# Kernel tuning notes

Measured on AMD Instinct MI355X. Metric: run time of the kernel, lower is better.

Reference implementation:

```python
import jax, jax.numpy as jnp
import numpy as np

THR = 0.2          # config['thr']
BORDER_RM = 2      # config['border_rm']
TEMP = 0.1         # config['dsmax_temperature']


def setup_inputs() -> dict:
    key = jax.random.key(0)
    k0, k1 = jax.random.split(key)
    N, C = 2, 256
    h0c, w0c, h1c, w1c = 60, 80, 60, 80
    return {
        "feat_c0": jax.random.normal(k0, (N, h0c * w0c, C), dtype=jnp.float32),
        "feat_c1": jax.random.normal(k1, (N, h1c * w1c, C), dtype=jnp.float32),
        "h0c": h0c, "w0c": w0c, "h1c": h1c, "w1c": w1c,
    }


def _valid_1d(n: int, b: int):
    # True in the interior [b, n-b), False on the border — matches mask_border writes
    return jnp.zeros((n,), dtype=bool).at[b:n - b].set(True)


def reference(feat_c0, feat_c1, h0c, w0c, h1c, w1c):
    N, L, C = feat_c0.shape
    S = feat_c1.shape[1]
    scale = 1.0 / (C ** 0.5)
    f0 = feat_c0 * scale
    f1 = feat_c1 * scale

    # similarity + dual softmax  -> conf_matrix [N, L, S]
    sim = jnp.einsum('nlc,nsc->nls', f0, f1) / TEMP
    conf = jax.nn.softmax(sim, axis=1) * jax.nn.softmax(sim, axis=2)

    # threshold + border removal (mask_border, vectorized as an interior mask)
    mask = conf > THR
    b = BORDER_RM
    border = (_valid_1d(h0c, b)[:, None, None, None]
              & _valid_1d(w0c, b)[None, :, None, None]
              & _valid_1d(h1c, b)[None, None, :, None]
              & _valid_1d(w1c, b)[None, None, None, :])  # [h0c,w0c,h1c,w1c]
    mask = (mask.reshape(N, h0c, w0c, h1c, w1c) & border[None]).reshape(N, L, S)

    # mutual nearest neighbor
    mask = mask \
        & (conf == conf.max(axis=2, keepdims=True)) \
        & (conf == conf.max(axis=1, keepdims=True))

    # match extraction, expressed densely (static shapes for jit):
    # mask_v[b,i] = row i of pair b has a match; j_ids its column; mconf its confidence
    mask_v = mask.any(axis=2)                               # [N, L]
    j_ids = jnp.argmax(mask, axis=2)                        # [N, L] (first True)
    mconf = jnp.take_along_axis(conf, j_ids[:, :, None], axis=2)[..., 0]
    mconf = jnp.where(mask_v, mconf, 0.0)                   # [N, L]

    # coarse keypoint coords for matched columns: (x, y) = (j % w1c, j // w1c)
    mkpts1_c = jnp.stack([j_ids % w1c, j_ids // w1c], axis=-1)  # [N, L, 2]

    return conf, mask_v, j_ids, mkpts1_c, mconf
```

## Files before the change

### kernel.cpp

```cpp
#include <hip/hip_runtime.h>

typedef _Float16 half8 __attribute__((ext_vector_type(8)));
typedef float f32x4 __attribute__((ext_vector_type(4)));

#define NB 2
#define LS 4800
#define CCH 256
#define W0 80
#define W1 80
#define THRV 0.2f
#define SQS 0.19764235376052370f

#define TN  38
#define TNM 19
#define PADL 4864
#define NWG (TN * TNM * NB)

#define OF_RST  0
#define OF_CST  19200
#define OF_RWM  38400
#define OF_CAND 48000
#define OF_CLM  57600
#define OF_PROW 67200
#define OF_PCOL (67200 + 739328)
#define OF_AH   (67200 + 2*739328)
#define OF_BH   (OF_AH + 1228800)

#define O_MASKV 46080000ull
#define O_JIDS  46089600ull
#define O_MKPT  46099200ull
#define O_MCONF 46118400ull

__device__ __forceinline__ void load_lds16(const void* g, void* l) {
    __builtin_amdgcn_global_load_lds((const __attribute__((address_space(1))) void*)g,
                                     (__attribute__((address_space(3))) void*)l, 16, 0, 0);
}

__device__ __forceinline__ void swizzle_ids(int& n, int& by, int& bx) {
    const int orig = ((int)blockIdx.z * TNM + (int)blockIdx.y) * TN + (int)blockIdx.x;
    const int xcd = orig & 7, t = orig >> 3;
    const int wg = (xcd < 4 ? xcd * 181 : 724 + (xcd - 4) * 180) + t;
    n = wg / (TN * TNM);
    const int rem = wg % (TN * TNM);
    by = rem / TN; bx = rem % TN;
}

__global__ __launch_bounds__(256) void conv_half(const float* __restrict__ A,
                                                 const float* __restrict__ B,
                                                 float* __restrict__ ws) {
    const int which = blockIdx.y;
    const float* src = which ? B : A;
    _Float16* dst = (_Float16*)(ws + (which ? OF_BH : OF_AH));
    const int idx = blockIdx.x * 256 + threadIdx.x;
    const float4 v = ((const float4*)src)[idx];
    union { _Float16 h[4]; uint2 u; } p;
    p.h[0] = (_Float16)(v.x * SQS);
    p.h[1] = (_Float16)(v.y * SQS);
    p.h[2] = (_Float16)(v.z * SQS);
    p.h[3] = (_Float16)(v.w * SQS);
    ((uint2*)dst)[idx] = p.u;
}

__device__ __forceinline__ void gemm_core(const _Float16* __restrict__ Ah,
                                          const _Float16* __restrict__ Bh,
                                          _Float16* smA, _Float16* smB,
                                          const int bx, const int by,
                                          const int tid, f32x4 (&acc)[4][4]) {
    const int lane = tid & 63, w = tid >> 6;
    const int wx = w & 1, wy = w >> 1;
    const int m = lane & 15, quad = lane >> 4;
    const int rr = lane >> 2;
    const int q = (lane & 3) ^ ((lane >> 3) & 3);

    const _Float16* ga[2];
    const _Float16* gb0;
    {
#pragma unroll
        for (int i = 0; i < 2; i++) {
            const int c = w * 2 + i;
            int gra = by * 256 + c * 16 + rr; gra = gra < LS ? gra : LS - 1;
            ga[i] = Ah + (size_t)gra * CCH + q * 8;
        }
        int grb = bx * 128 + w * 16 + rr; grb = grb < LS ? grb : LS - 1;
        gb0 = Bh + (size_t)grb * CCH + q * 8;
    }

#pragma unroll
    for (int i = 0; i < 2; i++) load_lds16(ga[i], &smA[(w * 2 + i) * 512]);
    load_lds16(gb0, &smB[w * 512]);

    for (int kt = 0; kt < 8; kt++) {
        __syncthreads();
        const int curA = (kt & 1) * 8192, curB = (kt & 1) * 4096;
        if (kt < 7) {
            const int ko = (kt + 1) * 32;
#pragma unroll
            for (int i = 0; i < 2; i++)
                load_lds16(ga[i] + ko, &smA[(8192 - curA) + (w * 2 + i) * 512]);
            load_lds16(gb0 + ko, &smB[(4096 - curB) + w * 512]);
        }
        half8 Af[4], Bf[4];
#pragma unroll
        for (int a = 0; a < 4; a++) {
            const int rl = wy * 64 + a * 16 + m;
            const int sl = rl * 4 + (quad ^ ((rl >> 1) & 3));
            Af[a] = *(const half8*)&smA[curA + sl * 8];
        }
#pragma unroll
        for (int b = 0; b < 4; b++) {
            const int cl = wx * 64 + b * 16 + m;
            const int sl = cl * 4 + (quad ^ ((cl >> 1) & 3));
            Bf[b] = *(const half8*)&smB[curB + sl * 8];
        }
#pragma unroll
        for (int a = 0; a < 4; a++)
#pragma unroll
            for (int b = 0; b < 4; b++)
                acc[a][b] = __builtin_amdgcn_mfma_f32_16x16x32_f16(Af[a], Bf[b], acc[a][b], 0, 0, 0);
    }
    __syncthreads();
}

__global__ __launch_bounds__(512, 4) void gemm_stats(float* __restrict__ ws) {
    __shared__ __align__(16) union {
        struct { _Float16 A[2][8192]; _Float16 B[2][4096]; } st;
        struct { float rs[256][2][2]; float cs[128][4][2]; } red;
    } sm;
    int n, by, bx;
    swizzle_ids(n, by, bx);
    const _Float16* Ah = (const _Float16*)(ws + OF_AH) + (size_t)n * LS * CCH;
    const _Float16* Bh = (const _Float16*)(ws + OF_BH) + (size_t)n * LS * CCH;
    const int tid = threadIdx.x;
    const int lane = tid & 63, w = tid >> 6;
    const int wx = w & 1, wy = w >> 1;
    const int m = lane & 15, quad = lane >> 4;

    f32x4 acc[4][4];
    {
        f32x4 z = {0.f, 0.f, 0.f, 0.f};
#pragma unroll
        for (int a = 0; a < 4; a++)
#pragma unroll
            for (int b = 0; b < 4; b++) acc[a][b] = z;
    }
    gemm_core(Ah, Bh, &sm.st.A[0][0], &sm.st.B[0][0], bx, by, tid, acc);

    const int l0 = by * 256, s0 = bx * 128;
    bool bval[4];
#pragma unroll
    for (int b = 0; b < 4; b++) bval[b] = (s0 + wx * 64 + b * 16 + m) < LS;

    float T = -1e30f;
#pragma unroll
    for (int a = 0; a < 4; a++)
#pragma unroll
        for (int reg = 0; reg < 4; reg++) {
            if ((l0 + wy * 64 + a * 16 + quad * 4 + reg) < LS) {
#pragma unroll
                for (int b = 0; b < 4; b++)
                    if (bval[b]) T = fmaxf(T, acc[a][b][reg]);
            }
        }
#pragma unroll
    for (int d = 1; d < 64; d <<= 1) T = fmaxf(T, __shfl_xor(T, d, 64));

#pragma unroll
    for (int a = 0; a < 4; a++)
#pragma unroll
        for (int reg = 0; reg < 4; reg++) {
            const bool rv = (l0 + wy * 64 + a * 16 + quad * 4 + reg) < LS;
#pragma unroll
            for (int b = 0; b < 4; b++)
                acc[a][b][reg] = (rv && bval[b]) ? __expf(acc[a][b][reg] - T) : 0.f;
        }

#pragma unroll
    for (int a = 0; a < 4; a++)
#pragma unroll
        for (int reg = 0; reg < 4; reg++) {
            float s = acc[a][0][reg] + acc[a][1][reg] + acc[a][2][reg] + acc[a][3][reg];
#pragma unroll
            for (int d = 1; d < 16; d <<= 1) s += __shfl_xor(s, d, 64);
            if (m == 0) {
                const int rl = wy * 64 + a * 16 + quad * 4 + reg;
                sm.red.rs[rl][wx][0] = T; sm.red.rs[rl][wx][1] = s;
            }
        }
#pragma unroll
    for (int b = 0; b < 4; b++) {
        float s = 0.f;
#pragma unroll
        for (int a = 0; a < 4; a++)
#pragma unroll
            for (int reg = 0; reg < 4; reg++) s += acc[a][b][reg];
        s += __shfl_xor(s, 16, 64);
        s += __shfl_xor(s, 32, 64);
        if (quad == 0) {
            const int cl = wx * 64 + b * 16 + m;
            sm.red.cs[cl][wy][0] = T; sm.red.cs[cl][wy][1] = s;
        }
    }
    __syncthreads();
    if (tid < 256) {
        const float m0 = sm.red.rs[tid][0][0], v0 = sm.red.rs[tid][0][1];
        const float m1 = sm.red.rs[tid][1][0], v1 = sm.red.rs[tid][1][1];
        const float nm = fmaxf(m0, m1);
        const float s = v0 * __expf(m0 - nm) + v1 * __expf(m1 - nm);
        ((float2*)(ws + OF_PROW))[((size_t)n * PADL + l0 + tid) * TN + bx] = make_float2(nm, s);
    } else if (tid < 384) {
        const int t = tid - 256;
        float M = sm.red.cs[t][0][0], S = sm.red.cs[t][0][1];
#pragma unroll
        for (int k = 1; k < 4; k++) {
            const float mo = sm.red.cs[t][k][0], so = sm.red.cs[t][k][1];
            const float nm = fmaxf(M, mo);
            S = S * __expf(M - nm) + so * __expf(mo - nm);
            M = nm;
        }
        ((float2*)(ws + OF_PCOL))[((size_t)n * PADL + s0 + t) * TNM + by] = make_float2(M, S);
    }
}

__global__ __launch_bounds__(256) void combine_stats(float* __restrict__ ws) {
    const int idx = blockIdx.x * 256 + threadIdx.x;
    const int half_ = idx >= 9600;
    const int i = idx - half_ * 9600;
    const int n = i / LS, r = i % LS;
    float M = -1e30f, S = 0.f;
    if (!half_) {
        const float2* P = (const float2*)(ws + OF_PROW) + ((size_t)n * PADL + r) * TN;
        for (int b = 0; b < TN; b++) {
            const float2 p = P[b];
            const float nm = fmaxf(M, p.x);
            S = S * __expf(M - nm) + p.y * __expf(p.x - nm);
            M = nm;
        }
        ((float2*)(ws + OF_RST))[n * LS + r] = make_float2(M, 1.0f / S);
    } else {
        const float2* P = (const float2*)(ws + OF_PCOL) + ((size_t)n * PADL + r) * TNM;
        for (int b = 0; b < TNM; b++) {
            const float2 p = P[b];
            const float nm = fmaxf(M, p.x);
            S = S * __expf(M - nm) + p.y * __expf(p.x - nm);
            M = nm;
        }
        ((float2*)(ws + OF_CST))[n * LS + r] = make_float2(M, 1.0f / S);
    }
}

__global__ __launch_bounds__(512, 4) void gemm_conf(float* __restrict__ out,
                                                    float* __restrict__ ws) {
    __shared__ __align__(16) union {
        struct { _Float16 A[2][8192]; _Float16 B[2][4096]; } st;
        struct { float rst[256][2]; float cst[128][2];
                 float rsv[256][2][2]; float csv[128][4]; } ep;
    } sm;
    int n, by, bx;
    swizzle_ids(n, by, bx);
    const _Float16* Ah = (const _Float16*)(ws + OF_AH) + (size_t)n * LS * CCH;
    const _Float16* Bh = (const _Float16*)(ws + OF_BH) + (size_t)n * LS * CCH;
    const int tid = threadIdx.x;
    const int lane = tid & 63, w = tid >> 6;
    const int wx = w & 1, wy = w >> 1;
    const int m = lane & 15, quad = lane >> 4;

    f32x4 acc[4][4];
    {
        f32x4 z = {0.f, 0.f, 0.f, 0.f};
#pragma unroll
        for (int a = 0; a < 4; a++)
#pragma unroll
            for (int b = 0; b < 4; b++) acc[a][b] = z;
    }
    gemm_core(Ah, Bh, &sm.st.A[0][0], &sm.st.B[0][0], bx, by, tid, acc);

    const int l0 = by * 256, s0 = bx * 128;
    if (tid < 256) {
        int r = l0 + tid; r = r < LS ? r : LS - 1;
        const float2 v = ((const float2*)(ws + OF_RST))[n * LS + r];
        sm.ep.rst[tid][0] = v.x; sm.ep.rst[tid][1] = v.y;
    } else if (tid < 384) {
        const int t = tid - 256;
        int c = s0 + t; c = c < LS ? c : LS - 1;
        const float2 v = ((const float2*)(ws + OF_CST))[n * LS + c];
        sm.ep.cst[t][0] = v.x; sm.ep.cst[t][1] = v.y;
    }
    __syncthreads();

    float* On = out + (size_t)n * LS * LS;
    float colm[4] = {-1.f, -1.f, -1.f, -1.f};
    bool bval[4]; int gc4[4]; float cmx[4], csi[4];
#pragma unroll
    for (int b = 0; b < 4; b++) {
        const int cl = wx * 64 + b * 16 + m;
        gc4[b] = s0 + cl;
        bval[b] = gc4[b] < LS;
        cmx[b] = sm.ep.cst[cl][0]; csi[b] = sm.ep.cst[cl][1];
    }
#pragma unroll
    for (int a = 0; a < 4; a++) {
#pragma unroll
        for (int reg = 0; reg < 4; reg++) {
            const int rl = wy * 64 + a * 16 + quad * 4 + reg;
            const int gr = l0 + rl;
            const float rm = sm.ep.rst[rl][0], rsi = sm.ep.rst[rl][1];
            const bool rv = gr < LS;
            float bestv = -1.f; int besti = 0;
#pragma unroll
            for (int b = 0; b < 4; b++) {
                const float c = __expf(2.f * acc[a][b][reg] - rm - cmx[b]) * (rsi * csi[b]);
                if (rv && bval[b]) {
                    __builtin_nontemporal_store(c, &On[(size_t)gr * LS + gc4[b]]);
                    if (c > bestv) { bestv = c; besti = gc4[b]; }
                    colm[b] = fmaxf(colm[b], c);
                }
            }
#pragma unroll
            for (int d = 1; d < 16; d <<= 1) {
                const float ov = __shfl_xor(bestv, d, 64);
                const int oi = __shfl_xor(besti, d, 64);
                if (ov > bestv || (ov == bestv && oi < besti)) { bestv = ov; besti = oi; }
            }
            if (m == 0) {
                sm.ep.rsv[rl][wx][0] = bestv;
                sm.ep.rsv[rl][wx][1] = __int_as_float(besti);
            }
        }
    }
#pragma unroll
    for (int b = 0; b < 4; b++) {
        float v = colm[b];
        v = fmaxf(v, __shfl_xor(v, 16, 64));
        v = fmaxf(v, __shfl_xor(v, 32, 64));
        if (quad == 0) sm.ep.csv[wx * 64 + b * 16 + m][wy] = v;
    }
    __syncthreads();
    if (tid < 256) {
        const float v0 = sm.ep.rsv[tid][0][0]; const int i0 = __float_as_int(sm.ep.rsv[tid][0][1]);
        const float v1 = sm.ep.rsv[tid][1][0]; const int i1 = __float_as_int(sm.ep.rsv[tid][1][1]);
        float bv; int bi;
        if (v0 > v1 || (v0 == v1 && i0 <= i1)) { bv = v0; bi = i0; } else { bv = v1; bi = i1; }
        ((float2*)(ws + OF_PROW))[((size_t)n * PADL + l0 + tid) * TN + bx] =
            make_float2(bv, __int_as_float(bi));
    } else if (tid < 384) {
        const int t = tid - 256;
        const float v = fmaxf(fmaxf(sm.ep.csv[t][0], sm.ep.csv[t][1]),
                              fmaxf(sm.ep.csv[t][2], sm.ep.csv[t][3]));
        (ws + OF_PCOL)[((size_t)n * PADL + s0 + t) * TNM + by] = v;
    }
}

__global__ __launch_bounds__(256) void combine_max(float* __restrict__ ws) {
    const int idx = blockIdx.x * 256 + threadIdx.x;
    const int half_ = idx >= 9600;
    const int i = idx - half_ * 9600;
    const int n = i / LS, r = i % LS;
    if (!half_) {
        const float2* P = (const float2*)(ws + OF_PROW) + ((size_t)n * PADL + r) * TN;
        float bv = -2.f; int bi = 0;
        for (int b = 0; b < TN; b++) {
            const float2 p = P[b];
            const int pi = __float_as_int(p.y);
            if (p.x > bv || (p.x == bv && pi < bi)) { bv = p.x; bi = pi; }
        }
        ws[OF_RWM + i] = bv;
        ((int*)ws)[OF_CAND + i] = bi;
    } else {
        const float* P = ws + OF_PCOL + ((size_t)n * PADL + r) * TNM;
        float v = -2.f;
        for (int b = 0; b < TNM; b++) v = fmaxf(v, P[b]);
        ws[OF_CLM + i] = v;
    }
}

__global__ __launch_bounds__(256) void match_pass(const float* __restrict__ ws,
                                                  float* __restrict__ out) {
    const int idx = blockIdx.x * 256 + threadIdx.x;
    if (idx >= NB * LS) return;
    const int n = idx / LS, l = idx % LS;
    const float rwm = ws[OF_RWM + idx];
    const int cand = ((const int*)ws)[OF_CAND + idx];
    const float clm = ws[OF_CLM + n * LS + cand];
    const int y0 = l / W0, x0 = l % W0;
    const int y1 = cand / W1, x1 = cand % W1;
    const bool b0 = (y0 >= 2 && y0 < 58 && x0 >= 2 && x0 < 78);
    const bool b1 = (y1 >= 2 && y1 < 58 && x1 >= 2 && x1 < 78);
    const bool matched = (rwm > THRV) && b0 && b1 && (rwm == clm);
    const int j = matched ? cand : 0;
    out[O_MASKV + idx] = matched ? 1.f : 0.f;
    out[O_JIDS + idx] = (float)j;
    out[O_MKPT + (size_t)idx * 2 + 0] = (float)(j % W1);
    out[O_MKPT + (size_t)idx * 2 + 1] = (float)(j / W1);
    out[O_MCONF + idx] = matched ? rwm : 0.f;
}

extern "C" void kernel_launch(void* const* d_in, const int* in_sizes, int n_in,
                              void* d_out, int out_size, void* d_ws, size_t ws_size,
                              hipStream_t stream) {
    const float* f0 = (const float*)d_in[0];
    const float* f1 = (const float*)d_in[1];
    float* out = (float*)d_out;
    float* ws = (float*)d_ws;

    conv_half<<<dim3(2400, 2), 256, 0, stream>>>(f0, f1, ws);
    gemm_stats<<<dim3(TN, TNM, NB), 512, 0, stream>>>(ws);
    combine_stats<<<75, 256, 0, stream>>>(ws);
    gemm_conf<<<dim3(TN, TNM, NB), 512, 0, stream>>>(out, ws);
    combine_max<<<75, 256, 0, stream>>>(ws);
    match_pass<<<38, 256, 0, stream>>>(ws, out);
}
```

Baseline: 310.6 us.

## Store raw similarity once and stream-normalize instead of recomputing GEMM

Drops the second GEMM pass. The first GEMM now writes raw similarity logits into the output buffer, and a new streaming kernel reads them back, applies the dual-softmax normalization in place, and computes per-row argmax and per-block column maxima. A simpler column-combine kernel replaces the old partial-max combine. The trade is cheaper compute for an extra full read and write of the 4800x4800 fp32 matrix per batch. The streaming kernel also runs on only 300 blocks, which may limit achievable bandwidth.

```diff
diff --git a/kernel.cpp b/kernel.cpp
--- a/kernel.cpp
+++ b/kernel.cpp
@@ -14,7 +14,8 @@
 #define TN  38
 #define TNM 19
 #define PADL 4864
-#define NWG (TN * TNM * NB)
+#define NROWB 32
+#define NPB   150
 
 #define OF_RST  0
 #define OF_CST  19200
@@ -23,6 +24,7 @@
 #define OF_CLM  57600
 #define OF_PROW 67200
 #define OF_PCOL (67200 + 739328)
+#define OF_CMAXP OF_PROW
 #define OF_AH   (67200 + 2*739328)
 #define OF_BH   (OF_AH + 1228800)
 
@@ -121,7 +123,8 @@
     __syncthreads();
 }
 
-__global__ __launch_bounds__(512, 4) void gemm_stats(float* __restrict__ ws) {
+__global__ __launch_bounds__(512, 4) void gemm_sim(float* __restrict__ out,
+                                                   float* __restrict__ ws) {
     __shared__ __align__(16) union {
         struct { _Float16 A[2][8192]; _Float16 B[2][4096]; } st;
         struct { float rs[256][2][2]; float cs[128][4][2]; } red;
@@ -146,9 +149,25 @@
     gemm_core(Ah, Bh, &sm.st.A[0][0], &sm.st.B[0][0], bx, by, tid, acc);
 
     const int l0 = by * 256, s0 = bx * 128;
-    bool bval[4];
-#pragma unroll
-    for (int b = 0; b < 4; b++) bval[b] = (s0 + wx * 64 + b * 16 + m) < LS;
+    bool bval[4]; int gc4[4];
+#pragma unroll
+    for (int b = 0; b < 4; b++) {
+        gc4[b] = s0 + wx * 64 + b * 16 + m;
+        bval[b] = gc4[b] < LS;
+    }
+
+    float* On = out + (size_t)n * LS * LS;
+#pragma unroll
+    for (int a = 0; a < 4; a++)
+#pragma unroll
+        for (int reg = 0; reg < 4; reg++) {
+            const int gr = l0 + wy * 64 + a * 16 + quad * 4 + reg;
+            if (gr < LS) {
+#pragma unroll
+                for (int b = 0; b < 4; b++)
+                    if (bval[b]) On[(size_t)gr * LS + gc4[b]] = acc[a][b][reg];
+            }
+        }
 
     float T = -1e30f;
 #pragma unroll
@@ -248,129 +267,86 @@
     }
 }
 
-__global__ __launch_bounds__(512, 4) void gemm_conf(float* __restrict__ out,
-                                                    float* __restrict__ ws) {
-    __shared__ __align__(16) union {
-        struct { _Float16 A[2][8192]; _Float16 B[2][4096]; } st;
-        struct { float rst[256][2]; float cst[128][2];
-                 float rsv[256][2][2]; float csv[128][4]; } ep;
-    } sm;
-    int n, by, bx;
-    swizzle_ids(n, by, bx);
-    const _Float16* Ah = (const _Float16*)(ws + OF_AH) + (size_t)n * LS * CCH;
-    const _Float16* Bh = (const _Float16*)(ws + OF_BH) + (size_t)n * LS * CCH;
+__global__ __launch_bounds__(256) void stream_conf(float* __restrict__ out,
+                                                   float* __restrict__ ws) {
+    const int n = blockIdx.y, rb = blockIdx.x;
     const int tid = threadIdx.x;
-    const int lane = tid & 63, w = tid >> 6;
-    const int wx = w & 1, wy = w >> 1;
-    const int m = lane & 15, quad = lane >> 4;
-
-    f32x4 acc[4][4];
-    {
-        f32x4 z = {0.f, 0.f, 0.f, 0.f};
-#pragma unroll
-        for (int a = 0; a < 4; a++)
-#pragma unroll
-            for (int b = 0; b < 4; b++) acc[a][b] = z;
-    }
-    gemm_core(Ah, Bh, &sm.st.A[0][0], &sm.st.B[0][0], bx, by, tid, acc);
-
-    const int l0 = by * 256, s0 = bx * 128;
-    if (tid < 256) {
-        int r = l0 + tid; r = r < LS ? r : LS - 1;
-        const float2 v = ((const float2*)(ws + OF_RST))[n * LS + r];
-        sm.ep.rst[tid][0] = v.x; sm.ep.rst[tid][1] = v.y;
-    } else if (tid < 384) {
-        const int t = tid - 256;
-        int c = s0 + t; c = c < LS ? c : LS - 1;
-        const float2 v = ((const float2*)(ws + OF_CST))[n * LS + c];
-        sm.ep.cst[t][0] = v.x; sm.ep.cst[t][1] = v.y;
-    }
-    __syncthreads();
-
-    float* On = out + (size_t)n * LS * LS;
-    float colm[4] = {-1.f, -1.f, -1.f, -1.f};
-    bool bval[4]; int gc4[4]; float cmx[4], csi[4];
-#pragma unroll
-    for (int b = 0; b < 4; b++) {
-        const int cl = wx * 64 + b * 16 + m;
-        gc4[b] = s0 + cl;
-        bval[b] = gc4[b] < LS;
-        cmx[b] = sm.ep.cst[cl][0]; csi[b] = sm.ep.cst[cl][1];
-    }
-#pragma unroll
-    for (int a = 0; a < 4; a++) {
-#pragma unroll
-        for (int reg = 0; reg < 4; reg++) {
-            const int rl = wy * 64 + a * 16 + quad * 4 + reg;
-            const int gr = l0 + rl;
-            const float rm = sm.ep.rst[rl][0], rsi = sm.ep.rst[rl][1];
-            const bool rv = gr < LS;
-            float bestv = -1.f; int besti = 0;
-#pragma unroll
-            for (int b = 0; b < 4; b++) {
-                const float c = __expf(2.f * acc[a][b][reg] - rm - cmx[b]) * (rsi * csi[b]);
-                if (rv && bval[b]) {
-                    __builtin_nontemporal_store(c, &On[(size_t)gr * LS + gc4[b]]);
-                    if (c > bestv) { bestv = c; besti = gc4[b]; }
-                    colm[b] = fmaxf(colm[b], c);
+    __shared__ float Lv[16][256];
+    __shared__ int   Li[16][256];
+    __shared__ float Mv[16][16];
+    __shared__ int   Mi[16][16];
+
+    float cmv[19], csiv[19], cmax[19];
+#pragma unroll
+    for (int j = 0; j < 19; j++) {
+        const int s = tid + j * 256;
+        cmax[j] = 0.f;
+        if (s < LS) {
+            const float2 v = ((const float2*)(ws + OF_CST))[n * LS + s];
+            cmv[j] = v.x; csiv[j] = v.y;
+        } else { cmv[j] = 0.f; csiv[j] = 0.f; }
+    }
+
+    float* base = out + ((size_t)n * LS + rb * NROWB) * LS;
+    for (int ch = 0; ch < 2; ch++) {
+        for (int r16 = 0; r16 < 16; r16++) {
+            const int r = ch * 16 + r16;
+            const float2 rs = ((const float2*)(ws + OF_RST))[n * LS + rb * NROWB + r];
+            float* row = base + (size_t)r * LS;
+            float lmax = -1.f; int lidx = 0;
+#pragma unroll
+            for (int j = 0; j < 19; j++) {
+                const int s = tid + j * 256;
+                if (s < LS) {
+                    const float x = row[s];
+                    const float c = __expf(2.f * x - rs.x - cmv[j]) * (rs.y * csiv[j]);
+                    __builtin_nontemporal_store(c, &row[s]);
+                    cmax[j] = fmaxf(cmax[j], c);
+                    if (c > lmax) { lmax = c; lidx = s; }
                 }
             }
-#pragma unroll
-            for (int d = 1; d < 16; d <<= 1) {
-                const float ov = __shfl_xor(bestv, d, 64);
-                const int oi = __shfl_xor(besti, d, 64);
-                if (ov > bestv || (ov == bestv && oi < besti)) { bestv = ov; besti = oi; }
-            }
-            if (m == 0) {
-                sm.ep.rsv[rl][wx][0] = bestv;
-                sm.ep.rsv[rl][wx][1] = __int_as_float(besti);
-            }
-        }
-    }
-#pragma unroll
-    for (int b = 0; b < 4; b++) {
-        float v = colm[b];
-        v = fmaxf(v, __shfl_xor(v, 16, 64));
-        v = fmaxf(v, __shfl_xor(v, 32, 64));
-        if (quad == 0) sm.ep.csv[wx * 64 + b * 16 + m][wy] = v;
-    }
-    __syncthreads();
-    if (tid < 256) {
-        const float v0 = sm.ep.rsv[tid][0][0]; const int i0 = __float_as_int(sm.ep.rsv[tid][0][1]);
-        const float v1 = sm.ep.rsv[tid][1][0]; const int i1 = __float_as_int(sm.ep.rsv[tid][1][1]);
-        float bv; int bi;
-        if (v0 > v1 || (v0 == v1 && i0 <= i1)) { bv = v0; bi = i0; } else { bv = v1; bi = i1; }
-        ((float2*)(ws + OF_PROW))[((size_t)n * PADL + l0 + tid) * TN + bx] =
-            make_float2(bv, __int_as_float(bi));
-    } else if (tid < 384) {
-        const int t = tid - 256;
-        const float v = fmaxf(fmaxf(sm.ep.csv[t][0], sm.ep.csv[t][1]),
-                              fmaxf(sm.ep.csv[t][2], sm.ep.csv[t][3]));
-        (ws + OF_PCOL)[((size_t)n * PADL + s0 + t) * TNM + by] = v;
-    }
-}
-
-__global__ __launch_bounds__(256) void combine_max(float* __restrict__ ws) {
+            Lv[r16][tid] = lmax; Li[r16][tid] = lidx;
+        }
+        __syncthreads();
+        {
+            const int r = tid >> 4, p = tid & 15;
+            float bv = -2.f; int bi = 0;
+            for (int k = 0; k < 16; k++) {
+                const float v = Lv[r][p * 16 + k]; const int ii = Li[r][p * 16 + k];
+                if (v > bv || (v == bv && ii < bi)) { bv = v; bi = ii; }
+            }
+            Mv[r][p] = bv; Mi[r][p] = bi;
+        }
+        __syncthreads();
+        if (tid < 16) {
+            float bv = -2.f; int bi = 0;
+            for (int p = 0; p < 16; p++) {
+                const float v = Mv[tid][p]; const int ii = Mi[tid][p];
+                if (v > bv || (v == bv && ii < bi)) { bv = v; bi = ii; }
+            }
+            const int gr = n * LS + rb * NROWB + ch * 16 + tid;
+            ws[OF_RWM + gr] = bv;
+            ((int*)ws)[OF_CAND + gr] = bi;
+        }
+        __syncthreads();
+    }
+
+#pragma unroll
+    for (int j = 0; j < 19; j++) {
+        const int s = tid + j * 256;
+        if (s < LS) ws[OF_CMAXP + ((size_t)n * NPB + rb) * LS + s] = cmax[j];
+    }
+}
+
+__global__ __launch_bounds__(256) void combine_col(float* __restrict__ ws) {
     const int idx = blockIdx.x * 256 + threadIdx.x;
-    const int half_ = idx >= 9600;
-    const int i = idx - half_ * 9600;
-    const int n = i / LS, r = i % LS;
-    if (!half_) {
-        const float2* P = (const float2*)(ws + OF_PROW) + ((size_t)n * PADL + r) * TN;
-        float bv = -2.f; int bi = 0;
-        for (int b = 0; b < TN; b++) {
-            const float2 p = P[b];
-            const int pi = __float_as_int(p.y);
-            if (p.x > bv || (p.x == bv && pi < bi)) { bv = p.x; bi = pi; }
-        }
-        ws[OF_RWM + i] = bv;
-        ((int*)ws)[OF_CAND + i] = bi;
-    } else {
-        const float* P = ws + OF_PCOL + ((size_t)n * PADL + r) * TNM;
-        float v = -2.f;
-        for (int b = 0; b < TNM; b++) v = fmaxf(v, P[b]);
-        ws[OF_CLM + i] = v;
-    }
+    if (idx >= NB * LS) return;
+    const int n = idx / LS, c = idx % LS;
+    const float* P = ws + OF_CMAXP + (size_t)n * NPB * LS + c;
+    float v = -2.f;
+#pragma unroll 4
+    for (int p = 0; p < NPB; p++) v = fmaxf(v, P[(size_t)p * LS]);
+    ws[OF_CLM + idx] = v;
 }
 
 __global__ __launch_bounds__(256) void match_pass(const float* __restrict__ ws,
@@ -403,9 +379,9 @@
     float* ws = (float*)d_ws;
 
     conv_half<<<dim3(2400, 2), 256, 0, stream>>>(f0, f1, ws);
-    gemm_stats<<<dim3(TN, TNM, NB), 512, 0, stream>>>(ws);
+    gemm_sim<<<dim3(TN, TNM, NB), 512, 0, stream>>>(out, ws);
     combine_stats<<<75, 256, 0, stream>>>(ws);
-    gemm_conf<<<dim3(TN, TNM, NB), 512, 0, stream>>>(out, ws);
-    combine_max<<<75, 256, 0, stream>>>(ws);
+    stream_conf<<<dim3(NPB, NB), 256, 0, stream>>>(out, ws);
+    combine_col<<<38, 256, 0, stream>>>(ws);
     match_pass<<<38, 256, 0, stream>>>(ws, out);
 }
```

Result: slower. 353.6 us (+13.8%).

## Restructure GEMM tiles to 64x128 with full-K LDS A and register-streamed B

Applied to the files above, without the earlier changes.

The GEMM tile changes from 256x128 to 64x128. The whole K extent of A is staged once in LDS, and each wave streams its B fragments straight from global memory into registers with a three-deep prefetch, which removes the per-k-step barriers and the B LDS staging. Column partial statistics now go into scratch space in the output buffer instead of workspace. The column max is reduced with atomicMax into a zeroed buffer, so the separate column-combine pass is dropped, and the non-temporal conf stores become plain stores. The smaller tile means four times as many workgroups and more redundant B reads per output element, in exchange for less synchronization and better occupancy.

```diff
diff --git a/kernel.cpp b/kernel.cpp
--- a/kernel.cpp
+++ b/kernel.cpp
@@ -11,10 +11,10 @@
 #define THRV 0.2f
 #define SQS 0.19764235376052370f
 
-#define TN  38
-#define TNM 19
-#define PADL 4864
-#define NWG (TN * TNM * NB)
+#define TBX 38
+#define TBY 75
+#define PIMG (TBX * TBY)
+#define NWG  (PIMG * NB)
 
 #define OF_RST  0
 #define OF_CST  19200
@@ -22,9 +22,8 @@
 #define OF_CAND 48000
 #define OF_CLM  57600
 #define OF_PROW 67200
-#define OF_PCOL (67200 + 739328)
-#define OF_AH   (67200 + 2*739328)
-#define OF_BH   (OF_AH + 1228800)
+#define OF_AH   796800
+#define OF_BH   2025600
 
 #define O_MASKV 46080000ull
 #define O_JIDS  46089600ull
@@ -37,12 +36,12 @@
 }
 
 __device__ __forceinline__ void swizzle_ids(int& n, int& by, int& bx) {
-    const int orig = ((int)blockIdx.z * TNM + (int)blockIdx.y) * TN + (int)blockIdx.x;
+    const int orig = ((int)blockIdx.z * TBY + (int)blockIdx.y) * TBX + (int)blockIdx.x;
     const int xcd = orig & 7, t = orig >> 3;
-    const int wg = (xcd < 4 ? xcd * 181 : 724 + (xcd - 4) * 180) + t;
-    n = wg / (TN * TNM);
-    const int rem = wg % (TN * TNM);
-    by = rem / TN; bx = rem % TN;
+    const int wg = (xcd < 4 ? xcd * 713 : 2852 + (xcd - 4) * 712) + t;
+    n = wg / PIMG;
+    const int rem = wg % PIMG;
+    by = rem / TBX; bx = rem % TBX;
 }
 
 __global__ __launch_bounds__(256) void conv_half(const float* __restrict__ A,
@@ -61,175 +60,181 @@
     ((uint2*)dst)[idx] = p.u;
 }
 
-__device__ __forceinline__ void gemm_core(const _Float16* __restrict__ Ah,
-                                          const _Float16* __restrict__ Bh,
-                                          _Float16* smA, _Float16* smB,
-                                          const int bx, const int by,
-                                          const int tid, f32x4 (&acc)[4][4]) {
-    const int lane = tid & 63, w = tid >> 6;
-    const int wx = w & 1, wy = w >> 1;
-    const int m = lane & 15, quad = lane >> 4;
-    const int rr = lane >> 2;
-    const int q = (lane & 3) ^ ((lane >> 3) & 3);
-
-    const _Float16* ga[2];
-    const _Float16* gb0;
-    {
-#pragma unroll
-        for (int i = 0; i < 2; i++) {
-            const int c = w * 2 + i;
-            int gra = by * 256 + c * 16 + rr; gra = gra < LS ? gra : LS - 1;
-            ga[i] = Ah + (size_t)gra * CCH + q * 8;
-        }
-        int grb = bx * 128 + w * 16 + rr; grb = grb < LS ? grb : LS - 1;
-        gb0 = Bh + (size_t)grb * CCH + q * 8;
-    }
-
-#pragma unroll
-    for (int i = 0; i < 2; i++) load_lds16(ga[i], &smA[(w * 2 + i) * 512]);
-    load_lds16(gb0, &smB[w * 512]);
-
+__device__ __forceinline__ void stage_A(const _Float16* __restrict__ Ah,
+                                        _Float16* smA, const int by, const int tid) {
+#pragma unroll
+    for (int i = 0; i < 4; i++) {
+        const int s = i * 512 + tid;
+        const int slice = s >> 8, rem = s & 255, row = rem >> 2, j = rem & 3;
+        const int q = j ^ ((row >> 1) & 3);
+        load_lds16(Ah + (size_t)(by * 64 + row) * CCH + slice * 32 + q * 8, smA + s * 8);
+    }
+}
+
+__device__ __forceinline__ void kloop(const _Float16* smA,
+                                      const _Float16* __restrict__ Bh,
+                                      const int colb, const int wrow,
+                                      const int m, const int quad,
+                                      f32x4 (&acc)[2][2]) {
+    const _Float16* bp0 = Bh + (size_t)(colb + m) * CCH + quad * 8;
+    const _Float16* bp1 = bp0 + 16 * CCH;
+    half8 Bs[3][2], Af[2][2];
+    Bs[0][0] = *(const half8*)bp0;
+    Bs[0][1] = *(const half8*)bp1;
+    Bs[1][0] = *(const half8*)(bp0 + 32);
+    Bs[1][1] = *(const half8*)(bp1 + 32);
+#pragma unroll
+    for (int a = 0; a < 2; a++) {
+        const int rl = wrow * 32 + a * 16 + m;
+        const int sl = rl * 4 + (quad ^ ((rl >> 1) & 3));
+        Af[0][a] = *(const half8*)&smA[sl * 8];
+    }
+#pragma unroll
     for (int kt = 0; kt < 8; kt++) {
-        __syncthreads();
-        const int curA = (kt & 1) * 8192, curB = (kt & 1) * 4096;
+        if (kt < 6) {
+            Bs[(kt + 2) % 3][0] = *(const half8*)(bp0 + (kt + 2) * 32);
+            Bs[(kt + 2) % 3][1] = *(const half8*)(bp1 + (kt + 2) * 32);
+        }
         if (kt < 7) {
-            const int ko = (kt + 1) * 32;
-#pragma unroll
-            for (int i = 0; i < 2; i++)
-                load_lds16(ga[i] + ko, &smA[(8192 - curA) + (w * 2 + i) * 512]);
-            load_lds16(gb0 + ko, &smB[(4096 - curB) + w * 512]);
-        }
-        half8 Af[4], Bf[4];
-#pragma unroll
-        for (int a = 0; a < 4; a++) {
-            const int rl = wy * 64 + a * 16 + m;
-            const int sl = rl * 4 + (quad ^ ((rl >> 1) & 3));
-            Af[a] = *(const half8*)&smA[curA + sl * 8];
-        }
-#pragma unroll
-        for (int b = 0; b < 4; b++) {
-            const int cl = wx * 64 + b * 16 + m;
-            const int sl = cl * 4 + (quad ^ ((cl >> 1) & 3));
-            Bf[b] = *(const half8*)&smB[curB + sl * 8];
-        }
-#pragma unroll
-        for (int a = 0; a < 4; a++)
-#pragma unroll
-            for (int b = 0; b < 4; b++)
-                acc[a][b] = __builtin_amdgcn_mfma_f32_16x16x32_f16(Af[a], Bf[b], acc[a][b], 0, 0, 0);
-    }
-    __syncthreads();
-}
-
-__global__ __launch_bounds__(512, 4) void gemm_stats(float* __restrict__ ws) {
-    __shared__ __align__(16) union {
-        struct { _Float16 A[2][8192]; _Float16 B[2][4096]; } st;
-        struct { float rs[256][2][2]; float cs[128][4][2]; } red;
-    } sm;
+#pragma unroll
+            for (int a = 0; a < 2; a++) {
+                const int rl = wrow * 32 + a * 16 + m;
+                const int sl = (kt + 1) * 256 + rl * 4 + (quad ^ ((rl >> 1) & 3));
+                Af[(kt + 1) & 1][a] = *(const half8*)&smA[sl * 8];
+            }
+        }
+#pragma unroll
+        for (int a = 0; a < 2; a++)
+#pragma unroll
+            for (int b = 0; b < 2; b++)
+                acc[a][b] = __builtin_amdgcn_mfma_f32_16x16x32_f16(Af[kt & 1][a], Bs[kt % 3][b], acc[a][b], 0, 0, 0);
+    }
+}
+
+__global__ __launch_bounds__(512, 4) void gemm_stats(float* __restrict__ out,
+                                                     float* __restrict__ ws) {
+    __shared__ __align__(16) _Float16 smA[16384];
+    __shared__ float rs[64][4][2];
+    __shared__ float cs[128][2][2];
     int n, by, bx;
     swizzle_ids(n, by, bx);
     const _Float16* Ah = (const _Float16*)(ws + OF_AH) + (size_t)n * LS * CCH;
     const _Float16* Bh = (const _Float16*)(ws + OF_BH) + (size_t)n * LS * CCH;
     const int tid = threadIdx.x;
     const int lane = tid & 63, w = tid >> 6;
-    const int wx = w & 1, wy = w >> 1;
+    const int wrow = w >> 2, wcol = w & 3;
     const int m = lane & 15, quad = lane >> 4;
 
-    f32x4 acc[4][4];
+    stage_A(Ah, smA, by, tid);
+    __syncthreads();
+
+    const int colb = bx * 128 + wcol * 32;
+    const bool bvalid = colb < LS;
+    f32x4 acc[2][2];
     {
         f32x4 z = {0.f, 0.f, 0.f, 0.f};
-#pragma unroll
-        for (int a = 0; a < 4; a++)
-#pragma unroll
-            for (int b = 0; b < 4; b++) acc[a][b] = z;
-    }
-    gemm_core(Ah, Bh, &sm.st.A[0][0], &sm.st.B[0][0], bx, by, tid, acc);
-
-    const int l0 = by * 256, s0 = bx * 128;
-    bool bval[4];
-#pragma unroll
-    for (int b = 0; b < 4; b++) bval[b] = (s0 + wx * 64 + b * 16 + m) < LS;
-
-    float T = -1e30f;
-#pragma unroll
-    for (int a = 0; a < 4; a++)
-#pragma unroll
-        for (int reg = 0; reg < 4; reg++) {
-            if ((l0 + wy * 64 + a * 16 + quad * 4 + reg) < LS) {
-#pragma unroll
-                for (int b = 0; b < 4; b++)
-                    if (bval[b]) T = fmaxf(T, acc[a][b][reg]);
+        acc[0][0] = z; acc[0][1] = z; acc[1][0] = z; acc[1][1] = z;
+    }
+    if (bvalid) {
+        kloop(smA, Bh, colb, wrow, m, quad, acc);
+
+        float T = -1e30f;
+#pragma unroll
+        for (int a = 0; a < 2; a++)
+#pragma unroll
+            for (int b = 0; b < 2; b++)
+#pragma unroll
+                for (int reg = 0; reg < 4; reg++) T = fmaxf(T, acc[a][b][reg]);
+#pragma unroll
+        for (int d = 1; d < 64; d <<= 1) T = fmaxf(T, __shfl_xor(T, d, 64));
+
+#pragma unroll
+        for (int a = 0; a < 2; a++)
+#pragma unroll
+            for (int b = 0; b < 2; b++)
+#pragma unroll
+                for (int reg = 0; reg < 4; reg++)
+                    acc[a][b][reg] = __expf(acc[a][b][reg] - T);
+
+#pragma unroll
+        for (int a = 0; a < 2; a++)
+#pragma unroll
+            for (int reg = 0; reg < 4; reg++) {
+                float s = acc[a][0][reg] + acc[a][1][reg];
+#pragma unroll
+                for (int d = 1; d < 16; d <<= 1) s += __shfl_xor(s, d, 64);
+                if (m == 0) {
+                    const int rl = wrow * 32 + a * 16 + quad * 4 + reg;
+                    rs[rl][wcol][0] = T; rs[rl][wcol][1] = s;
+                }
             }
-        }
-#pragma unroll
-    for (int d = 1; d < 64; d <<= 1) T = fmaxf(T, __shfl_xor(T, d, 64));
-
-#pragma unroll
-    for (int a = 0; a < 4; a++)
-#pragma unroll
-        for (int reg = 0; reg < 4; reg++) {
-            const bool rv = (l0 + wy * 64 + a * 16 + quad * 4 + reg) < LS;
-#pragma unroll
-            for (int b = 0; b < 4; b++)
-                acc[a][b][reg] = (rv && bval[b]) ? __expf(acc[a][b][reg] - T) : 0.f;
-        }
-
-#pragma unroll
-    for (int a = 0; a < 4; a++)
-#pragma unroll
-        for (int reg = 0; reg < 4; reg++) {
-            float s = acc[a][0][reg] + acc[a][1][reg] + acc[a][2][reg] + acc[a][3][reg];
-#pragma unroll
-            for (int d = 1; d < 16; d <<= 1) s += __shfl_xor(s, d, 64);
-            if (m == 0) {
-                const int rl = wy * 64 + a * 16 + quad * 4 + reg;
-                sm.red.rs[rl][wx][0] = T; sm.red.rs[rl][wx][1] = s;
+#pragma unroll
+        for (int b = 0; b < 2; b++) {
+            float s = 0.f;
+#pragma unroll
+            for (int a = 0; a < 2; a++)
+#pragma unroll
+                for (int reg = 0; reg < 4; reg++) s += acc[a][b][reg];
+            s += __shfl_xor(s, 16, 64);
+            s += __shfl_xor(s, 32, 64);
+            if (quad == 0) {
+                const int cl = wcol * 32 + b * 16 + m;
+                cs[cl][wrow][0] = T; cs[cl][wrow][1] = s;
             }
         }
-#pragma unroll
-    for (int b = 0; b < 4; b++) {
-        float s = 0.f;
-#pragma unroll
-        for (int a = 0; a < 4; a++)
-#pragma unroll
-            for (int reg = 0; reg < 4; reg++) s += acc[a][b][reg];
-        s += __shfl_xor(s, 16, 64);
-        s += __shfl_xor(s, 32, 64);
+    } else {
+        if (m == 0) {
+#pragma unroll
+            for (int a = 0; a < 2; a++)
+#pragma unroll
+                for (int reg = 0; reg < 4; reg++) {
+                    const int rl = wrow * 32 + a * 16 + quad * 4 + reg;
+                    rs[rl][wcol][0] = -1e30f; rs[rl][wcol][1] = 0.f;
+                }
+        }
         if (quad == 0) {
-            const int cl = wx * 64 + b * 16 + m;
-            sm.red.cs[cl][wy][0] = T; sm.red.cs[cl][wy][1] = s;
+#pragma unroll
+            for (int b = 0; b < 2; b++) {
+                const int cl = wcol * 32 + b * 16 + m;
+                cs[cl][wrow][0] = -1e30f; cs[cl][wrow][1] = 0.f;
+            }
         }
     }
     __syncthreads();
-    if (tid < 256) {
-        const float m0 = sm.red.rs[tid][0][0], v0 = sm.red.rs[tid][0][1];
-        const float m1 = sm.red.rs[tid][1][0], v1 = sm.red.rs[tid][1][1];
-        const float nm = fmaxf(m0, m1);
-        const float s = v0 * __expf(m0 - nm) + v1 * __expf(m1 - nm);
-        ((float2*)(ws + OF_PROW))[((size_t)n * PADL + l0 + tid) * TN + bx] = make_float2(nm, s);
-    } else if (tid < 384) {
-        const int t = tid - 256;
-        float M = sm.red.cs[t][0][0], S = sm.red.cs[t][0][1];
-#pragma unroll
-        for (int k = 1; k < 4; k++) {
-            const float mo = sm.red.cs[t][k][0], so = sm.red.cs[t][k][1];
-            const float nm = fmaxf(M, mo);
-            S = S * __expf(M - nm) + so * __expf(mo - nm);
+    if (tid < 64) {
+        float M = -1e30f, S = 0.f;
+#pragma unroll
+        for (int k = 0; k < 4; k++) {
+            const float mk = rs[tid][k][0], sk = rs[tid][k][1];
+            const float nm = fmaxf(M, mk);
+            S = S * __expf(M - nm) + sk * __expf(mk - nm);
             M = nm;
         }
-        ((float2*)(ws + OF_PCOL))[((size_t)n * PADL + s0 + t) * TNM + by] = make_float2(M, S);
-    }
-}
-
-__global__ __launch_bounds__(256) void combine_stats(float* __restrict__ ws) {
+        ((float2*)(ws + OF_PROW))[((size_t)n * LS + by * 64 + tid) * TBX + bx] = make_float2(M, S);
+    } else if (tid < 192) {
+        const int c = tid - 64;
+        const int col = bx * 128 + c;
+        if (col < LS) {
+            float M = cs[c][0][0], S = cs[c][0][1];
+            const float mk = cs[c][1][0], sk = cs[c][1][1];
+            const float nm = fmaxf(M, mk);
+            S = S * __expf(M - nm) + sk * __expf(mk - nm);
+            M = nm;
+            ((float2*)out)[((size_t)n * LS + col) * TBY + by] = make_float2(M, S);
+        }
+    }
+}
+
+__global__ __launch_bounds__(256) void combine_stats(const float* __restrict__ out,
+                                                     float* __restrict__ ws) {
     const int idx = blockIdx.x * 256 + threadIdx.x;
     const int half_ = idx >= 9600;
     const int i = idx - half_ * 9600;
     const int n = i / LS, r = i % LS;
     float M = -1e30f, S = 0.f;
     if (!half_) {
-        const float2* P = (const float2*)(ws + OF_PROW) + ((size_t)n * PADL + r) * TN;
-        for (int b = 0; b < TN; b++) {
+        const float2* P = (const float2*)(ws + OF_PROW) + ((size_t)n * LS + r) * TBX;
+        for (int b = 0; b < TBX; b++) {
             const float2 p = P[b];
             const float nm = fmaxf(M, p.x);
             S = S * __expf(M - nm) + p.y * __expf(p.x - nm);
@@ -237,140 +242,136 @@
         }
         ((float2*)(ws + OF_RST))[n * LS + r] = make_float2(M, 1.0f / S);
     } else {
-        const float2* P = (const float2*)(ws + OF_PCOL) + ((size_t)n * PADL + r) * TNM;
-        for (int b = 0; b < TNM; b++) {
+        const float2* P = (const float2*)out + ((size_t)n * LS + r) * TBY;
+        for (int b = 0; b < TBY; b++) {
             const float2 p = P[b];
             const float nm = fmaxf(M, p.x);
             S = S * __expf(M - nm) + p.y * __expf(p.x - nm);
             M = nm;
         }
         ((float2*)(ws + OF_CST))[n * LS + r] = make_float2(M, 1.0f / S);
+        ws[OF_CLM + i] = 0.0f;
     }
 }
 
 __global__ __launch_bounds__(512, 4) void gemm_conf(float* __restrict__ out,
                                                     float* __restrict__ ws) {
-    __shared__ __align__(16) union {
-        struct { _Float16 A[2][8192]; _Float16 B[2][4096]; } st;
-        struct { float rst[256][2]; float cst[128][2];
-                 float rsv[256][2][2]; float csv[128][4]; } ep;
-    } sm;
+    __shared__ __align__(16) _Float16 smA[16384];
+    __shared__ float rsv[64][4][2];
+    __shared__ float csv[128][2];
     int n, by, bx;
     swizzle_ids(n, by, bx);
     const _Float16* Ah = (const _Float16*)(ws + OF_AH) + (size_t)n * LS * CCH;
     const _Float16* Bh = (const _Float16*)(ws + OF_BH) + (size_t)n * LS * CCH;
     const int tid = threadIdx.x;
     const int lane = tid & 63, w = tid >> 6;
-    const int wx = w & 1, wy = w >> 1;
+    const int wrow = w >> 2, wcol = w & 3;
     const int m = lane & 15, quad = lane >> 4;
 
-    f32x4 acc[4][4];
+    stage_A(Ah, smA, by, tid);
+    __syncthreads();
+
+    const int colb = bx * 128 + wcol * 32;
+    const bool bvalid = colb < LS;
+    f32x4 acc[2][2];
     {
         f32x4 z = {0.f, 0.f, 0.f, 0.f};
-#pragma unroll
-        for (int a = 0; a < 4; a++)
-#pragma unroll
-            for (int b = 0; b < 4; b++) acc[a][b] = z;
-    }
-    gemm_core(Ah, Bh, &sm.st.A[0][0], &sm.st.B[0][0], bx, by, tid, acc);
-
-    const int l0 = by * 256, s0 = bx * 128;
-    if (tid < 256) {
-        int r = l0 + tid; r = r < LS ? r : LS - 1;
-        const float2 v = ((const float2*)(ws + OF_RST))[n * LS + r];
-        sm.ep.rst[tid][0] = v.x; sm.ep.rst[tid][1] = v.y;
-    } else if (tid < 384) {
-        const int t = tid - 256;
-        int c = s0 + t; c = c < LS ? c : LS - 1;
-        const float2 v = ((const float2*)(ws + OF_CST))[n * LS + c];
-        sm.ep.cst[t][0] = v.x; sm.ep.cst[t][1] = v.y;
+        acc[0][0] = z; acc[0][1] = z; acc[1][0] = z; acc[1][1] = z;
+    }
+    if (bvalid) {
+        kloop(smA, Bh, colb, wrow, m, quad, acc);
+
+        float* On = out + (size_t)n * LS * LS;
+        float colm[2] = {-1.f, -1.f};
+        float cmx[2], csi[2];
+#pragma unroll
+        for (int b = 0; b < 2; b++) {
+            const float2 cv = ((const float2*)(ws + OF_CST))[n * LS + colb + b * 16 + m];
+            cmx[b] = cv.x; csi[b] = cv.y;
+        }
+#pragma unroll
+        for (int a = 0; a < 2; a++) {
+#pragma unroll
+            for (int reg = 0; reg < 4; reg++) {
+                const int rl = wrow * 32 + a * 16 + quad * 4 + reg;
+                const int gr = by * 64 + rl;
+                const float2 rv = ((const float2*)(ws + OF_RST))[n * LS + gr];
+                float bestv = -1.f; int besti = 0;
+#pragma unroll
+                for (int b = 0; b < 2; b++) {
+                    const float c = __expf(2.f * acc[a][b][reg] - rv.x - cmx[b]) * (rv.y * csi[b]);
+                    On[(size_t)gr * LS + colb + b * 16 + m] = c;
+                    if (c > bestv) { bestv = c; besti = colb + b * 16 + m; }
+                    colm[b] = fmaxf(colm[b], c);
+                }
+#pragma unroll
+                for (int d = 1; d < 16; d <<= 1) {
+                    const float ov = __shfl_xor(bestv, d, 64);
+                    const int oi = __shfl_xor(besti, d, 64);
+                    if (ov > bestv || (ov == bestv && oi < besti)) { bestv = ov; besti = oi; }
+                }
+                if (m == 0) {
+                    rsv[rl][wcol][0] = bestv;
+                    rsv[rl][wcol][1] = __int_as_float(besti);
+                }
+            }
+        }
+#pragma unroll
+        for (int b = 0; b < 2; b++) {
+            float v = colm[b];
+            v = fmaxf(v, __shfl_xor(v, 16, 64));
+            v = fmaxf(v, __shfl_xor(v, 32, 64));
+            if (quad == 0) csv[wcol * 32 + b * 16 + m][wrow] = v;
+        }
+    } else {
+        if (m == 0) {
+#pragma unroll
+            for (int a = 0; a < 2; a++)
+#pragma unroll
+                for (int reg = 0; reg < 4; reg++) {
+                    const int rl = wrow * 32 + a * 16 + quad * 4 + reg;
+                    rsv[rl][wcol][0] = -1.f; rsv[rl][wcol][1] = 0.f;
+                }
+        }
+        if (quad == 0) {
+#pragma unroll
+            for (int b = 0; b < 2; b++) csv[wcol * 32 + b * 16 + m][wrow] = -1.f;
+        }
     }
     __syncthreads();
-
-    float* On = out + (size_t)n * LS * LS;
-    float colm[4] = {-1.f, -1.f, -1.f, -1.f};
-    bool bval[4]; int gc4[4]; float cmx[4], csi[4];
-#pragma unroll
-    for (int b = 0; b < 4; b++) {
-        const int cl = wx * 64 + b * 16 + m;
-        gc4[b] = s0 + cl;
-        bval[b] = gc4[b] < LS;
-        cmx[b] = sm.ep.cst[cl][0]; csi[b] = sm.ep.cst[cl][1];
-    }
-#pragma unroll
-    for (int a = 0; a < 4; a++) {
-#pragma unroll
-        for (int reg = 0; reg < 4; reg++) {
-            const int rl = wy * 64 + a * 16 + quad * 4 + reg;
-            const int gr = l0 + rl;
-            const float rm = sm.ep.rst[rl][0], rsi = sm.ep.rst[rl][1];
-            const bool rv = gr < LS;
-            float bestv = -1.f; int besti = 0;
-#pragma unroll
-            for (int b = 0; b < 4; b++) {
-                const float c = __expf(2.f * acc[a][b][reg] - rm - cmx[b]) * (rsi * csi[b]);
-                if (rv && bval[b]) {
-                    __builtin_nontemporal_store(c, &On[(size_t)gr * LS + gc4[b]]);
-                    if (c > bestv) { bestv = c; besti = gc4[b]; }
-                    colm[b] = fmaxf(colm[b], c);
-                }
-            }
-#pragma unroll
-            for (int d = 1; d < 16; d <<= 1) {
-                const float ov = __shfl_xor(bestv, d, 64);
-                const int oi = __shfl_xor(besti, d, 64);
-                if (ov > bestv || (ov == bestv && oi < besti)) { bestv = ov; besti = oi; }
-            }
-            if (m == 0) {
-                sm.ep.rsv[rl][wx][0] = bestv;
-                sm.ep.rsv[rl][wx][1] = __int_as_float(besti);
-            }
-        }
-    }
-#pragma unroll
-    for (int b = 0; b < 4; b++) {
-        float v = colm[b];
-        v = fmaxf(v, __shfl_xor(v, 16, 64));
-        v = fmaxf(v, __shfl_xor(v, 32, 64));
-        if (quad == 0) sm.ep.csv[wx * 64 + b * 16 + m][wy] = v;
-    }
-    __syncthreads();
-    if (tid < 256) {
-        const float v0 = sm.ep.rsv[tid][0][0]; const int i0 = __float_as_int(sm.ep.rsv[tid][0][1]);
-        const float v1 = sm.ep.rsv[tid][1][0]; const int i1 = __float_as_int(sm.ep.rsv[tid][1][1]);
-        float bv; int bi;
-        if (v0 > v1 || (v0 == v1 && i0 <= i1)) { bv = v0; bi = i0; } else { bv = v1; bi = i1; }
-        ((float2*)(ws + OF_PROW))[((size_t)n * PADL + l0 + tid) * TN + bx] =
+    if (tid < 64) {
+        float bv = -2.f; int bi = 0;
+#pragma unroll
+        for (int k = 0; k < 4; k++) {
+            const float v = rsv[tid][k][0]; const int ii = __float_as_int(rsv[tid][k][1]);
+            if (v > bv || (v == bv && ii < bi)) { bv = v; bi = ii; }
+        }
+        ((float2*)(ws + OF_PROW))[((size_t)n * LS + by * 64 + tid) * TBX + bx] =
             make_float2(bv, __int_as_float(bi));
-    } else if (tid < 384) {
-        const int t = tid - 256;
-        const float v = fmaxf(fmaxf(sm.ep.csv[t][0], sm.ep.csv[t][1]),
-                              fmaxf(sm.ep.csv[t][2], sm.ep.csv[t][3]));
-        (ws + OF_PCOL)[((size_t)n * PADL + s0 + t) * TNM + by] = v;
+    } else if (tid < 192) {
+        const int c = tid - 64;
+        const int col = bx * 128 + c;
+        if (col < LS) {
+            const float v = fmaxf(csv[c][0], csv[c][1]);
+            if (v > 0.f)
+                atomicMax((int*)(ws + OF_CLM) + n * LS + col, __float_as_int(v));
+        }
     }
 }
 
 __global__ __launch_bounds__(256) void combine_max(float* __restrict__ ws) {
-    const int idx = blockIdx.x * 256 + threadIdx.x;
-    const int half_ = idx >= 9600;
-    const int i = idx - half_ * 9600;
+    const int i = blockIdx.x * 256 + threadIdx.x;
+    if (i >= NB * LS) return;
     const int n = i / LS, r = i % LS;
-    if (!half_) {
-        const float2* P = (const float2*)(ws + OF_PROW) + ((size_t)n * PADL + r) * TN;
-        float bv = -2.f; int bi = 0;
-        for (int b = 0; b < TN; b++) {
-            const float2 p = P[b];
-            const int pi = __float_as_int(p.y);
-            if (p.x > bv || (p.x == bv && pi < bi)) { bv = p.x; bi = pi; }
-        }
-        ws[OF_RWM + i] = bv;
-        ((int*)ws)[OF_CAND + i] = bi;
-    } else {
-        const float* P = ws + OF_PCOL + ((size_t)n * PADL + r) * TNM;
-        float v = -2.f;
-        for (int b = 0; b < TNM; b++) v = fmaxf(v, P[b]);
-        ws[OF_CLM + i] = v;
-    }
+    const float2* P = (const float2*)(ws + OF_PROW) + ((size_t)n * LS + r) * TBX;
+    float bv = -2.f; int bi = 0;
+    for (int b = 0; b < TBX; b++) {
+        const float2 p = P[b];
+        const int pi = __float_as_int(p.y);
+        if (p.x > bv || (p.x == bv && pi < bi)) { bv = p.x; bi = pi; }
+    }
+    ws[OF_RWM + i] = bv;
+    ((int*)ws)[OF_CAND + i] = bi;
 }
 
 __global__ __launch_bounds__(256) void match_pass(const float* __restrict__ ws,
@@ -403,9 +404,9 @@
     float* ws = (float*)d_ws;
 
     conv_half<<<dim3(2400, 2), 256, 0, stream>>>(f0, f1, ws);
-    gemm_stats<<<dim3(TN, TNM, NB), 512, 0, stream>>>(ws);
-    combine_stats<<<75, 256, 0, stream>>>(ws);
-    gemm_conf<<<dim3(TN, TNM, NB), 512, 0, stream>>>(out, ws);
-    combine_max<<<75, 256, 0, stream>>>(ws);
+    gemm_stats<<<dim3(TBX, TBY, NB), 512, 0, stream>>>(out, ws);
+    combine_stats<<<75, 256, 0, stream>>>(out, ws);
+    gemm_conf<<<dim3(TBX, TBY, NB), 512, 0, stream>>>(out, ws);
+    combine_max<<<38, 256, 0, stream>>>(ws);
     match_pass<<<38, 256, 0, stream>>>(ws, out);
 }
```

Result: slower. 405.6 us (+30.6%).
